# Optimization experiments

Measured on AMD Instinct MI355X. Metric: run time of the kernel, lower is better.

## Reference

```python
import jax, jax.numpy as jnp
import numpy as np


def _dwconv(x, w, b):
    # depthwise conv, NCHW, kernel [C,1,k,k], SAME padding k//2
    k = w.shape[-1]
    p = k // 2
    out = jax.lax.conv_general_dilated(x, w, (1, 1), [(p, p), (p, p)],
                                       feature_group_count=x.shape[1])
    return out + b[None, :, None, None]


def _conv1x1(x, W, b):
    return jnp.einsum('oc,bchw->bohw', W, x) + b[None, :, None, None]


def _ca_weight(q, k):
    # q,k: [b,c,h,w] -> energy [b,h,w,h+w]
    eH = jnp.einsum('bchw,bcgw->bhwg', q, k)  # attend along H (column)
    eW = jnp.einsum('bchw,bchv->bhwv', q, k)  # attend along W (row)
    return jnp.concatenate([eH, eW], axis=3)


def _ca_map(att, v):
    # att: [b,h,w,h+w], v: [b,c,h,w]
    h = v.shape[2]
    outH = jnp.einsum('bcgw,bhwg->bchw', v, att[..., :h])
    outW = jnp.einsum('bchv,bhwv->bchw', v, att[..., h:])
    return outH + outW


def _cc_block(cnn, Wq, bq, Wk, bk, Wv, bv, gamma):
    q = _conv1x1(cnn, Wq, bq)
    k = _conv1x1(cnn, Wk, bk)
    v = _conv1x1(cnn, Wv, bv)
    att = jax.nn.softmax(_ca_weight(q, k), axis=1)  # softmax over H axis, as in torch F.softmax(energy, 1)
    return gamma * _ca_map(att, v) + cnn


def _ppeg(x, w7, b7, w5, b5, w3, b3, H, W):
    C = x.shape[1]
    cnn = x.T.reshape(1, C, H, W)
    out = _dwconv(cnn, w7, b7) + cnn + _dwconv(cnn, w5, b5) + _dwconv(cnn, w3, b3)
    return out.reshape(C, H * W).T  # [N, C]


def setup_inputs() -> dict:
    key = jax.random.key(0)
    N, DIM, HID, QK = 65536, 1024, 512, 64  # N = 256^2
    ks = jax.random.split(key, 26)
    s = 0.02
    inp = {
        'h0': jax.random.normal(ks[0], (N, DIM), jnp.float32),
        'w7': jax.random.normal(ks[1], (DIM, 1, 7, 7)) * s,
        'b7': jax.random.normal(ks[2], (DIM,)) * s,
        'w5': jax.random.normal(ks[3], (DIM, 1, 5, 5)) * s,
        'b5': jax.random.normal(ks[4], (DIM,)) * s,
        'w3': jax.random.normal(ks[5], (DIM, 1, 3, 3)) * s,
        'b3': jax.random.normal(ks[6], (DIM,)) * s,
        'W1': jax.random.normal(ks[7], (HID, DIM)) * s,
        'b1': jax.random.normal(ks[8], (HID,)) * s,
        'Wq': jax.random.normal(ks[9], (QK, HID)) * s,
        'bq': jax.random.normal(ks[10], (QK,)) * s,
        'Wk': jax.random.normal(ks[11], (QK, HID)) * s,
        'bk': jax.random.normal(ks[12], (QK,)) * s,
        'Wv': jax.random.normal(ks[13], (HID, HID)) * s,
        'bv': jax.random.normal(ks[14], (HID,)) * s,
        'gamma': jax.random.normal(ks[15], ()) * 0.5,
        'Wq1': jax.random.normal(ks[16], (QK, HID)) * s,
        'bq1': jax.random.normal(ks[17], (QK,)) * s,
        'Wk1': jax.random.normal(ks[18], (QK, HID)) * s,
        'bk1': jax.random.normal(ks[19], (QK,)) * s,
        'Wv1': jax.random.normal(ks[20], (HID, HID)) * s,
        'bv1': jax.random.normal(ks[21], (HID,)) * s,
        'gamma1': jax.random.normal(ks[22], ()) * 0.5,
        'Wfc': jax.random.normal(ks[23], (1, HID)) * s,
        'bfc': jax.random.normal(ks[24], (1,)) * s,
    }
    return inp


def reference(h0, w7, b7, w5, b5, w3, b3, W1, b1,
              Wq, bq, Wk, bk, Wv, bv, gamma,
              Wq1, bq1, Wk1, bk1, Wv1, bv1, gamma1, Wfc, bfc):
    N = h0.shape[0]
    side = int(np.ceil(np.sqrt(N)))
    pad = side * side - N
    h1 = jnp.concatenate([h0, h0[:pad]], axis=0) if pad > 0 else h0
    # PPEG positional encoding (multi-kernel depthwise conv)
    h1 = _ppeg(h1, w7, b7, w5, b5, w3, b3, side, side)
    # fc1: Linear(1024->512) + ReLU  (h1 already square -> second pad is no-op)
    h2 = jax.nn.relu(h1 @ W1.T + b1)  # [N, 512]
    # CCAttention (two criss-cross blocks + fc to 1 logit)
    cnn = h2.T.reshape(1, h2.shape[1], side, side)
    out = _cc_block(cnn, Wq, bq, Wk, bk, Wv, bv, gamma)
    out1 = _cc_block(out, Wq1, bq1, Wk1, bk1, Wv1, bv1, gamma1)
    out1 = out1.reshape(out1.shape[1], side * side).T  # [N, 512]
    logits = out1 @ Wfc.T + bfc  # [N, 1]
    A = jax.nn.softmax(logits.T, axis=1)  # [1, N] attention over instances
    return A
```

## Files before the change

kernel.cpp:

```cpp
#include <hip/hip_runtime.h>

#define HW 65536
#define SIDE 256

typedef __attribute__((ext_vector_type(8))) short short8v;
typedef __attribute__((ext_vector_type(4))) float f32x4;
typedef __attribute__((ext_vector_type(8))) ushort ushort8v;

__device__ __forceinline__ ushort f2bf(float f) {
  unsigned int u = __builtin_bit_cast(unsigned int, f);
  u = (u + 0x7fff + ((u >> 16) & 1)) >> 16;
  return (ushort)u;
}
__device__ __forceinline__ float bf2f(unsigned int u) {
  return __builtin_bit_cast(float, (u & 0xffffu) << 16);
}
__device__ __forceinline__ float bflo(unsigned int d) {
  return __builtin_bit_cast(float, d << 16);
}
__device__ __forceinline__ float bfhi(unsigned int d) {
  return __builtin_bit_cast(float, d & 0xffff0000u);
}
__device__ __forceinline__ void gld16(const void* g, void* l) {
  __builtin_amdgcn_global_load_lds(
      (const __attribute__((address_space(1))) void*)g,
      (__attribute__((address_space(3))) void*)l, 16, 0, 0);
}

__global__ __launch_bounds__(256) void k_prep(
    const float* __restrict__ W1, const float* __restrict__ Wv,
    const float* __restrict__ Wv1, const float* __restrict__ Wq,
    const float* __restrict__ Wk, const float* __restrict__ Wq1,
    const float* __restrict__ Wk1, const float* __restrict__ bq,
    const float* __restrict__ bk, const float* __restrict__ bq1,
    const float* __restrict__ bk1, const float* __restrict__ w7,
    const float* __restrict__ b7, const float* __restrict__ w5,
    const float* __restrict__ b5, const float* __restrict__ w3,
    const float* __restrict__ b3,
    ushort* __restrict__ W1b, ushort* __restrict__ Wvb,
    ushort* __restrict__ Wv1b, ushort* __restrict__ Wqkb,
    ushort* __restrict__ Wqk1b, float* __restrict__ bqk,
    float* __restrict__ bqk1, float* __restrict__ wc, float* __restrict__ bc) {
  const int i = blockIdx.x * 256 + threadIdx.x;
  if (i < 524288) { W1b[i] = f2bf(W1[i]); return; }
  if (i < 786432) { int j = i - 524288; Wvb[j] = f2bf(Wv[j]); return; }
  if (i < 1048576) { int j = i - 786432; Wv1b[j] = f2bf(Wv1[j]); return; }
  if (i < 1081344) { int j = i - 1048576; Wqkb[j] = f2bf(Wq[j]); return; }
  if (i < 1114112) { int j = i - 1081344; Wqkb[32768 + j] = f2bf(Wk[j]); return; }
  if (i < 1146880) { int j = i - 1114112; Wqk1b[j] = f2bf(Wq1[j]); return; }
  if (i < 1179648) { int j = i - 1146880; Wqk1b[32768 + j] = f2bf(Wk1[j]); return; }
  if (i < 1179904) {
    int j = i - 1179648;
    if (j < 64) bqk[j] = bq[j];
    else if (j < 128) bqk[j] = bk[j - 64];
    else if (j < 192) bqk1[j - 128] = bq1[j - 128];
    else bqk1[j - 128] = bk1[j - 192];
    return;
  }
  if (i < 1180928) {
    const int c = i - 1179904;
    float w[49];
#pragma unroll
    for (int t = 0; t < 49; t++) w[t] = w7[c * 49 + t];
    for (int dy = 0; dy < 5; dy++)
      for (int dx = 0; dx < 5; dx++)
        w[(dy + 1) * 7 + (dx + 1)] += w5[c * 25 + dy * 5 + dx];
    for (int dy = 0; dy < 3; dy++)
      for (int dx = 0; dx < 3; dx++)
        w[(dy + 2) * 7 + (dx + 2)] += w3[c * 9 + dy * 3 + dx];
    w[3 * 7 + 3] += 1.0f;
#pragma unroll
    for (int t = 0; t < 49; t++) wc[c * 49 + t] = w[t];
    bc[c] = b7[c] + b5[c] + b3[c];
  }
}

__global__ __launch_bounds__(256) void k_transpose_nc_v(
    const float* __restrict__ in, ushort* __restrict__ out) {
  __shared__ ushort t[64][64];
  const int c0 = blockIdx.x << 6, r0 = blockIdx.y << 6;
  const int tid = threadIdx.x;
#pragma unroll
  for (int p = 0; p < 2; p++) {
    const int r = (tid >> 3) + p * 32, c8 = tid & 7;
    const float4 f0 = *(const float4*)&in[(size_t)(r0 + r) * 1024 + c0 + c8 * 8];
    const float4 f1 = *(const float4*)&in[(size_t)(r0 + r) * 1024 + c0 + c8 * 8 + 4];
    ushort8v v;
    v[0] = f2bf(f0.x); v[1] = f2bf(f0.y); v[2] = f2bf(f0.z); v[3] = f2bf(f0.w);
    v[4] = f2bf(f1.x); v[5] = f2bf(f1.y); v[6] = f2bf(f1.z); v[7] = f2bf(f1.w);
    *(ushort8v*)&t[r][(c8 ^ ((r >> 3) & 7)) * 8] = v;
  }
  __syncthreads();
#pragma unroll
  for (int p = 0; p < 2; p++) {
    const int c = (tid >> 3) + p * 32, r8 = tid & 7;
    ushort8v v;
#pragma unroll
    for (int j = 0; j < 8; j++) {
      const int rr = r8 * 8 + j;
      v[j] = t[rr][(((c >> 3) ^ r8) << 3) + (c & 7)];
    }
    *(ushort8v*)&out[(size_t)(c0 + c) * HW + r0 + r8 * 8] = v;
  }
}

__global__ __launch_bounds__(256) void k_trv(const ushort* __restrict__ in,
    ushort* __restrict__ out, int R, int C, long long bs) {
  __shared__ ushort t[64][64];
  const size_t base = (size_t)blockIdx.z * bs;
  const int c0 = blockIdx.x << 6, r0 = blockIdx.y << 6;
  const int tid = threadIdx.x;
#pragma unroll
  for (int p = 0; p < 2; p++) {
    const int r = (tid >> 3) + p * 32, c8 = tid & 7;
    const ushort8v v = *(const ushort8v*)&in[base + (size_t)(r0 + r) * C + c0 + c8 * 8];
    *(ushort8v*)&t[r][(c8 ^ ((r >> 3) & 7)) * 8] = v;
  }
  __syncthreads();
#pragma unroll
  for (int p = 0; p < 2; p++) {
    const int c = (tid >> 3) + p * 32, r8 = tid & 7;
    ushort8v v;
#pragma unroll
    for (int j = 0; j < 8; j++) {
      const int rr = r8 * 8 + j;
      v[j] = t[rr][(((c >> 3) ^ r8) << 3) + (c & 7)];
    }
    *(ushort8v*)&out[base + (size_t)(c0 + c) * R + r0 + r8 * 8] = v;
  }
}

__global__ __launch_bounds__(256) void k_dwconv7(const ushort* __restrict__ X,
    const float* __restrict__ wc, const float* __restrict__ bc,
    ushort* __restrict__ out) {
  __shared__ ushort tile[38][272];
  const int c = blockIdx.y;
  const int y0 = blockIdx.x << 5;
  const int tid = threadIdx.x;
  const ushort* Xc = X + (size_t)c * HW;

  float w[49];
#pragma unroll
  for (int i = 0; i < 49; i++) w[i] = wc[c * 49 + i];
  const float bcv = bc[c];

  if (tid < 76) {
    const int r = tid >> 1;
    ushort8v z = {0, 0, 0, 0, 0, 0, 0, 0};
    *(ushort8v*)&tile[r][(tid & 1) ? 264 : 0] = z;
  }
  for (int i = tid; i < 38 * 32; i += 256) {
    const int r = i >> 5, j8 = i & 31;
    const int y = y0 - 3 + r;
    ushort8v v = {0, 0, 0, 0, 0, 0, 0, 0};
    if (y >= 0 && y < SIDE) v = *(const ushort8v*)&Xc[y * SIDE + j8 * 8];
    *(ushort8v*)&tile[r][8 + j8 * 8] = v;
  }
  __syncthreads();

  const int t0 = tid & 63;
  const int ry = (tid >> 6) << 3;
  float acc[8][4] = {};
#pragma unroll
  for (int r = 0; r < 14; r++) {
    const uint2 ua = *(const uint2*)&tile[ry + r][(t0 << 2) + 4];
    const uint2 ub = *(const uint2*)&tile[ry + r][(t0 << 2) + 8];
    const uint2 uc = *(const uint2*)&tile[ry + r][(t0 << 2) + 12];
    float rv[12];
    rv[0] = bflo(ua.x); rv[1] = bfhi(ua.x); rv[2] = bflo(ua.y); rv[3] = bfhi(ua.y);
    rv[4] = bflo(ub.x); rv[5] = bfhi(ub.x); rv[6] = bflo(ub.y); rv[7] = bfhi(ub.y);
    rv[8] = bflo(uc.x); rv[9] = bfhi(uc.x); rv[10] = bflo(uc.y); rv[11] = bfhi(uc.y);
#pragma unroll
    for (int m = 0; m < 8; m++) {
      const int dy = r - m;
      if (dy < 0 || dy > 6) continue;
#pragma unroll
      for (int dx = 0; dx < 7; dx++) {
        const float ww = w[dy * 7 + dx];
#pragma unroll
        for (int o = 0; o < 4; o++) acc[m][o] += ww * rv[o + 1 + dx];
      }
    }
  }
#pragma unroll
  for (int m = 0; m < 8; m++) {
    ushort4 o4 = {f2bf(acc[m][0] + bcv), f2bf(acc[m][1] + bcv),
                  f2bf(acc[m][2] + bcv), f2bf(acc[m][3] + bcv)};
    *(ushort4*)&out[(size_t)c * HW + (y0 + ry + m) * SIDE + (t0 << 2)] = o4;
  }
}

template <int K, int RELU, int TRN>
__global__ __launch_bounds__(512) void k_mm8(
    const ushort* __restrict__ A, int lda,
    const ushort* __restrict__ B, int ldb,
    const float* __restrict__ bias,
    ushort* __restrict__ Cb, int ldc,
    ushort* __restrict__ Ct, int ldt) {
  constexpr int NT = K / 32;
  __shared__ __align__(16) ushort SM[2 * 12288];
  const int tid = threadIdx.x;
  const int lane = tid & 63, wv = tid >> 6;

  const int id = blockIdx.x;
  const int wg = (id & 7) * 128 + (id >> 3);
  const int bm = (wg >> 9) << 8;
  const int bn = (wg & 511) << 7;

  const int l4 = lane >> 2;
  const int sch = (lane & 3) ^ (l4 & 3);
  const int rA0 = (wv * 2) * 16 + l4;
  const int rA1 = (wv * 2 + 1) * 16 + l4;
  const int rB = wv * 16 + l4;
  const ushort* ApS0 = A + (size_t)(bm + rA0) * lda + sch * 8;
  const ushort* ApS1 = A + (size_t)(bm + rA1) * lda + sch * 8;
  const ushort* BpS = B + (size_t)(bn + rB) * ldb + sch * 8;
  const int dA0 = (wv * 2) * 512 + lane * 8;
  const int dA1 = (wv * 2 + 1) * 512 + lane * 8;
  const int dB = wv * 512 + lane * 8;

  const int wm = wv & 3, wn = wv >> 2;
  const int fr = lane & 15, kq = lane >> 4;
  int offA[4], offB[4];
#pragma unroll
  for (int mi = 0; mi < 4; mi++) {
    const int row = wm * 64 + mi * 16 + fr;
    offA[mi] = row * 32 + ((kq ^ (row & 3)) << 3);
  }
#pragma unroll
  for (int ni = 0; ni < 4; ni++) {
    const int row = wn * 64 + ni * 16 + fr;
    offB[ni] = 8192 + row * 32 + ((kq ^ (row & 3)) << 3);
  }

  f32x4 acc[4][4];
#pragma unroll
  for (int mi = 0; mi < 4; mi++)
#pragma unroll
    for (int ni = 0; ni < 4; ni++) acc[mi][ni] = (f32x4){0.f, 0.f, 0.f, 0.f};

#define STAGE8(bufbase, k0)                         \
  do {                                              \
    gld16(ApS0 + (k0), &SM[(bufbase) + dA0]);       \
    gld16(ApS1 + (k0), &SM[(bufbase) + dA1]);       \
    gld16(BpS + (k0), &SM[(bufbase) + 8192 + dB]);  \
  } while (0)

  STAGE8(0, 0);
  STAGE8(12288, 32);
  asm volatile("s_waitcnt vmcnt(3)" ::: "memory");
  __builtin_amdgcn_s_barrier();

  int cur = 0;
#pragma unroll 2
  for (int t = 0; t < NT; ++t) {
    const int base = cur ? 12288 : 0;
    short8v a[4], b2[4];
#pragma unroll
    for (int mi = 0; mi < 4; mi++) a[mi] = *(const short8v*)&SM[base + offA[mi]];
#pragma unroll
    for (int ni = 0; ni < 4; ni++) b2[ni] = *(const short8v*)&SM[base + offB[ni]];
    asm volatile("s_waitcnt lgkmcnt(0)" ::: "memory");
    __builtin_amdgcn_s_barrier();
    const int ts = (t + 2 < NT) ? (t + 2) : (NT - 1);
    STAGE8(base, ts << 5);
    __builtin_amdgcn_s_setprio(1);
#pragma unroll
    for (int mi = 0; mi < 4; mi++)
#pragma unroll
      for (int ni = 0; ni < 4; ni++)
        acc[mi][ni] = __builtin_amdgcn_mfma_f32_16x16x32_bf16(b2[ni], a[mi], acc[mi][ni], 0, 0, 0);
    __builtin_amdgcn_s_setprio(0);
    asm volatile("s_waitcnt vmcnt(3)" ::: "memory");
    __builtin_amdgcn_s_barrier();
    cur ^= 1;
  }
#undef STAGE8
  asm volatile("s_waitcnt vmcnt(0)" ::: "memory");
  __builtin_amdgcn_s_barrier();

  ushort tb[4][4][4];
#pragma unroll
  for (int mi = 0; mi < 4; mi++) {
    const int row = bm + wm * 64 + mi * 16 + fr;
    const float bs1 = bias[row];
#pragma unroll
    for (int ni = 0; ni < 4; ni++) {
      const int col = bn + wn * 64 + ni * 16 + (kq << 2);
      float4 v;
      v.x = acc[mi][ni][0] + bs1; v.y = acc[mi][ni][1] + bs1;
      v.z = acc[mi][ni][2] + bs1; v.w = acc[mi][ni][3] + bs1;
      if (RELU) {
        v.x = fmaxf(v.x, 0.f); v.y = fmaxf(v.y, 0.f);
        v.z = fmaxf(v.z, 0.f); v.w = fmaxf(v.w, 0.f);
      }
      const ushort4 u = {f2bf(v.x), f2bf(v.y), f2bf(v.z), f2bf(v.w)};
      *(ushort4*)&Cb[(size_t)row * ldc + col] = u;
      if (TRN) {
        tb[mi][ni][0] = u.x; tb[mi][ni][1] = u.y;
        tb[mi][ni][2] = u.z; tb[mi][ni][3] = u.w;
      }
    }
  }

  if constexpr (TRN) {
    ushort* St = SM;
#pragma unroll
    for (int hh = 0; hh < 2; hh++) {
      __builtin_amdgcn_s_barrier();
      if (wn == hh) {
#pragma unroll
        for (int mi = 0; mi < 4; mi++) {
          const int cl = wm * 64 + mi * 16 + fr;
#pragma unroll
          for (int ni = 0; ni < 4; ni++) {
            const int nl = ni * 16 + (kq << 2);
#pragma unroll
            for (int r = 0; r < 4; r++) St[(nl + r) * 256 + cl] = tb[mi][ni][r];
          }
        }
      }
      __builtin_amdgcn_s_barrier();
      const int cid = tid * 4;
      const int rowo = cid >> 5;
#pragma unroll
      for (int j = 0; j < 4; j++) {
        const int ch = (cid + j) & 31;
        const ushort8v vv = *(const ushort8v*)&St[rowo * 256 + ch * 8];
        *(ushort8v*)&Ct[(size_t)(bn + hh * 64 + rowo) * ldt + bm + ch * 8] = vv;
      }
    }
  }
}

template <int BN, int BIAS, int RELU, int OUTF, int OUTB, int SWZ>
__global__ __launch_bounds__(256) void k_mm(
    const ushort* __restrict__ A, int lda, long long bsA,
    const ushort* __restrict__ B, int ldb, long long bsB,
    const float* __restrict__ bias,
    float* __restrict__ Cf, ushort* __restrict__ Cb, int ldc, long long bsC,
    int K) {
  static_assert(BN == 64 || BN == 128, "BN");
  constexpr int FN = BN / 32;
  __shared__ __align__(16) ushort SMEM[128 * 32 + BN * 32];
  ushort* As = SMEM;
  ushort* Bs = SMEM + 128 * 32;
  const int tid = threadIdx.x;

  int bx, by, bz;
  if constexpr (SWZ == 0) {
    bx = blockIdx.x; by = blockIdx.y; bz = blockIdx.z;
  } else if constexpr (SWZ == 2) {
    const int id = blockIdx.x, l = id >> 3;
    bz = (id & 7) * 32 + (l >> 2); bx = l & 1; by = (l >> 1) & 1;
  } else {
    const int id = blockIdx.x, l = id >> 3;
    bz = (id & 7) * 32 + (l >> 3); bx = l & 3; by = (l >> 2) & 1;
  }

  const int bm = bx << 7, bn = by * BN;
  const long long zA = (long long)bz * bsA;
  const long long zB = (long long)bz * bsB;
  const long long zC = (long long)bz * bsC;

  const int sr = tid >> 2, sq = tid & 3;
  const int sw0 = (sr >> 1) & 3;
  const int sw1 = ((sr + 64) >> 1) & 3;
  const ushort* Ap0 = A + zA + (size_t)(bm + sr) * lda + ((sq ^ sw0) << 3);
  const ushort* Ap1 = A + zA + (size_t)(bm + sr + 64) * lda + ((sq ^ sw1) << 3);
  const ushort* Bp0 = B + zB + (size_t)(bn + sr) * ldb + ((sq ^ sw0) << 3);
  const ushort* Bp1 = nullptr;
  if constexpr (BN == 128)
    Bp1 = B + zB + (size_t)(bn + sr + 64) * ldb + ((sq ^ sw1) << 3);
  ushort* wA0 = &As[sr * 32 + sq * 8];
  ushort* wA1 = &As[(sr + 64) * 32 + sq * 8];
  ushort* wB0 = &Bs[sr * 32 + sq * 8];
  ushort* wB1 = nullptr;
  if constexpr (BN == 128) wB1 = &Bs[(sr + 64) * 32 + sq * 8];

  const int lane = tid & 63, wv = tid >> 6;
  const int wm = wv & 1, wn = wv >> 1;
  const int fr = lane & 15, kq = lane >> 4;
  int offA[4], offB[FN];
#pragma unroll
  for (int mi = 0; mi < 4; mi++) {
    const int row = wm * 64 + mi * 16 + fr;
    offA[mi] = row * 32 + ((kq ^ ((row >> 1) & 3)) << 3);
  }
#pragma unroll
  for (int ni = 0; ni < FN; ni++) {
    const int row = wn * (BN / 2) + ni * 16 + fr;
    offB[ni] = row * 32 + ((kq ^ ((row >> 1) & 3)) << 3);
  }

  f32x4 acc[4][FN];
#pragma unroll
  for (int mi = 0; mi < 4; mi++)
#pragma unroll
    for (int ni = 0; ni < FN; ni++) acc[mi][ni] = (f32x4){0.f, 0.f, 0.f, 0.f};

  for (int k0 = 0; k0 < K; k0 += 32) {
    __syncthreads();
    gld16(Ap0 + k0, wA0);
    gld16(Ap1 + k0, wA1);
    gld16(Bp0 + k0, wB0);
    if constexpr (BN == 128) gld16(Bp1 + k0, wB1);
    __syncthreads();
    short8v a[4], b[FN];
#pragma unroll
    for (int mi = 0; mi < 4; mi++) a[mi] = *(const short8v*)&As[offA[mi]];
#pragma unroll
    for (int ni = 0; ni < FN; ni++) b[ni] = *(const short8v*)&Bs[offB[ni]];
#pragma unroll
    for (int mi = 0; mi < 4; mi++)
#pragma unroll
      for (int ni = 0; ni < FN; ni++)
        acc[mi][ni] = __builtin_amdgcn_mfma_f32_16x16x32_bf16(b[ni], a[mi], acc[mi][ni], 0, 0, 0);
  }

#pragma unroll
  for (int mi = 0; mi < 4; mi++) {
    const int row = bm + wm * 64 + mi * 16 + fr;
    const float bs1 = (BIAS == 1) ? bias[row] : 0.f;
#pragma unroll
    for (int ni = 0; ni < FN; ni++) {
      const int col = bn + wn * (BN / 2) + ni * 16 + (kq << 2);
      float4 v;
      v.x = acc[mi][ni][0]; v.y = acc[mi][ni][1];
      v.z = acc[mi][ni][2]; v.w = acc[mi][ni][3];
      if (BIAS == 1) { v.x += bs1; v.y += bs1; v.z += bs1; v.w += bs1; }
      if (BIAS == 2) {
        const float4 bc4 = *(const float4*)&bias[col];
        v.x += bc4.x; v.y += bc4.y; v.z += bc4.z; v.w += bc4.w;
      }
      if (RELU) {
        v.x = fmaxf(v.x, 0.f); v.y = fmaxf(v.y, 0.f);
        v.z = fmaxf(v.z, 0.f); v.w = fmaxf(v.w, 0.f);
      }
      const size_t idx = (size_t)(zC + (size_t)row * ldc + col);
      if (OUTF) *(float4*)&Cf[idx] = v;
      if (OUTB) {
        ushort4 u = {f2bf(v.x), f2bf(v.y), f2bf(v.z), f2bf(v.w)};
        *(ushort4*)&Cb[idx] = u;
      }
    }
  }
}

__global__ __launch_bounds__(256) void k_energy(
    const ushort* __restrict__ A, int lda, long long bsA,
    const ushort* __restrict__ B, int ldb, long long bsB,
    ushort* __restrict__ E) {
  __shared__ __align__(16) ushort SA[128 * 64];
  __shared__ __align__(16) ushort SB[128 * 64];
  const int tid = threadIdx.x;
  const int id = blockIdx.x, l = id >> 3;
  const int bz = (id & 7) * 32 + (l >> 2), bx = l & 1, by = (l >> 1) & 1;
  const int bm = bx << 7, bn = by << 7;
  const long long zA = (long long)bz * bsA;
  const long long zB = (long long)bz * bsB;

#pragma unroll
  for (int j = 0; j < 4; j++) {
    const int g = j * 256 + tid;
    const int row = g >> 3, ch = g & 7;
    const int sc = ch ^ (row & 7);
    gld16(A + zA + (size_t)(bm + row) * lda + sc * 8, &SA[g * 8]);
    gld16(B + zB + (size_t)(bn + row) * ldb + sc * 8, &SB[g * 8]);
  }
  __syncthreads();

  const int lane = tid & 63, wv = tid >> 6;
  const int wm = wv & 1, wn = wv >> 1;
  const int fr = lane & 15, kq = lane >> 4;
  f32x4 acc[4][4];
#pragma unroll
  for (int mi = 0; mi < 4; mi++)
#pragma unroll
    for (int ni = 0; ni < 4; ni++) acc[mi][ni] = (f32x4){0.f, 0.f, 0.f, 0.f};

#pragma unroll
  for (int ks = 0; ks < 2; ks++) {
    short8v a[4], b[4];
#pragma unroll
    for (int mi = 0; mi < 4; mi++) {
      const int row = wm * 64 + mi * 16 + fr;
      a[mi] = *(const short8v*)&SA[row * 64 + (((ks * 4 + kq) ^ (row & 7)) << 3)];
    }
#pragma unroll
    for (int ni = 0; ni < 4; ni++) {
      const int row = wn * 64 + ni * 16 + fr;
      b[ni] = *(const short8v*)&SB[row * 64 + (((ks * 4 + kq) ^ (row & 7)) << 3)];
    }
#pragma unroll
    for (int mi = 0; mi < 4; mi++)
#pragma unroll
      for (int ni = 0; ni < 4; ni++)
        acc[mi][ni] = __builtin_amdgcn_mfma_f32_16x16x32_bf16(b[ni], a[mi], acc[mi][ni], 0, 0, 0);
  }

  const long long zC = (long long)bz * 65536;
#pragma unroll
  for (int mi = 0; mi < 4; mi++) {
    const int row = bm + wm * 64 + mi * 16 + fr;
#pragma unroll
    for (int ni = 0; ni < 4; ni++) {
      const int col = bn + wn * 64 + ni * 16 + (kq << 2);
      ushort4 u = {f2bf(acc[mi][ni][0]), f2bf(acc[mi][ni][1]),
                   f2bf(acc[mi][ni][2]), f2bf(acc[mi][ni][3])};
      *(ushort4*)&E[(size_t)(zC + (size_t)row * 256 + col)] = u;
    }
  }
}

__global__ __launch_bounds__(256) void k_softmax8(const ushort* __restrict__ EW,
    ushort* __restrict__ AW, const ushort* __restrict__ EH,
    ushort* __restrict__ AH) {
  __shared__ float sm[8][32], ss[8][32];
  const int b = blockIdx.x, tid = threadIdx.x;
  const int lc = tid & 31, seg = tid >> 5;
  const ushort* E;
  ushort* A;
  size_t base;
  int hs;
  if (b < 2048) {
    E = EW; A = AW; hs = HW;
    base = (size_t)b * 32 + lc;
  } else {
    E = EH; A = AH; hs = 256;
    const int cf = (b - 2048) * 32 + lc;
    base = (size_t)(cf >> 8) * HW + (cf & 255);
  }
  const size_t bh = base + (size_t)(seg * 32) * hs;
  float v[32];
#pragma unroll
  for (int h = 0; h < 32; h++) v[h] = bf2f(E[bh + (size_t)h * hs]);
  float m = v[0];
#pragma unroll
  for (int h = 1; h < 32; h++) m = fmaxf(m, v[h]);
  float s = 0.f;
#pragma unroll
  for (int h = 0; h < 32; h++) s += __expf(v[h] - m);
  sm[seg][lc] = m;
  ss[seg][lc] = s;
  __syncthreads();
  float M = sm[0][lc];
#pragma unroll
  for (int i = 1; i < 8; i++) M = fmaxf(M, sm[i][lc]);
  float S = 0.f;
#pragma unroll
  for (int i = 0; i < 8; i++) S += ss[i][lc] * __expf(sm[i][lc] - M);
  const float inv = 1.0f / S;
#pragma unroll
  for (int h = 0; h < 32; h++)
    A[bh + (size_t)h * hs] = f2bf(__expf(v[h] - M) * inv);
}

__global__ __launch_bounds__(256) void k_merge3(const ushort* __restrict__ O,
    const ushort* __restrict__ TH, const ushort* __restrict__ CN,
    const float* __restrict__ gammap, ushort* __restrict__ outB) {
  __shared__ ushort t[64][64];
  const float g = *gammap;
  const size_t base = (size_t)blockIdx.z * HW;
  const int h0 = blockIdx.y << 6, w0 = blockIdx.x << 6;
  const int tid = threadIdx.x;
#pragma unroll
  for (int p = 0; p < 2; p++) {
    const int r = (tid >> 3) + p * 32, c8 = tid & 7;
    const ushort8v v = *(const ushort8v*)&TH[base + (w0 + r) * SIDE + h0 + c8 * 8];
    *(ushort8v*)&t[r][(c8 ^ ((r >> 3) & 7)) * 8] = v;
  }
  __syncthreads();
#pragma unroll
  for (int p = 0; p < 2; p++) {
    const int h = (tid >> 3) + p * 32, r8 = tid & 7;
    const size_t idx = base + (h0 + h) * SIDE + w0 + r8 * 8;
    const ushort8v o8 = *(const ushort8v*)&O[idx];
    const ushort8v c8v = *(const ushort8v*)&CN[idx];
    ushort8v res;
#pragma unroll
    for (int j = 0; j < 8; j++) {
      const int rr = r8 * 8 + j;
      const float th = bf2f(t[rr][(((h >> 3) ^ r8) << 3) + (h & 7)]);
      res[j] = f2bf(g * (bf2f(o8[j]) + th) + bf2f(c8v[j]));
    }
    *(ushort8v*)&outB[idx] = res;
  }
}

__global__ __launch_bounds__(256) void k_logits2(const ushort* __restrict__ X,
    const float* __restrict__ Wfc, const float* __restrict__ bfc,
    float* __restrict__ L) {
  const int n0 = (blockIdx.x * 256 + threadIdx.x) * 2;
  float s0 = 0.f, s1 = 0.f;
  for (int j = 0; j < 512; j++) {
    const unsigned int u = *(const unsigned int*)&X[(size_t)j * HW + n0];
    const float wj = Wfc[j];
    s0 += bflo(u) * wj;
    s1 += bfhi(u) * wj;
  }
  float2 o = {s0 + bfc[0], s1 + bfc[0]};
  *(float2*)&L[n0] = o;
}

__global__ __launch_bounds__(256) void k_smax_reduce(const float* __restrict__ L,
                                                     float* __restrict__ red) {
  __shared__ float sm[256];
  const int tid = threadIdx.x;
  float m = -3.4e38f;
  for (int i = tid; i < HW; i += 256) m = fmaxf(m, L[i]);
  sm[tid] = m;
  __syncthreads();
  for (int s = 128; s > 0; s >>= 1) {
    if (tid < s) sm[tid] = fmaxf(sm[tid], sm[tid + s]);
    __syncthreads();
  }
  const float M = sm[0];
  __syncthreads();
  float sum = 0.f;
  for (int i = tid; i < HW; i += 256) sum += expf(L[i] - M);
  sm[tid] = sum;
  __syncthreads();
  for (int s = 128; s > 0; s >>= 1) {
    if (tid < s) sm[tid] += sm[tid + s];
    __syncthreads();
  }
  if (tid == 0) { red[0] = M; red[1] = sm[0]; }
}

__global__ __launch_bounds__(256) void k_smax_write(const float* __restrict__ L,
    const float* __restrict__ red, float* __restrict__ out) {
  const int n = blockIdx.x * 256 + threadIdx.x;
  out[n] = expf(L[n] - red[0]) * (1.0f / red[1]);
}

extern "C" void kernel_launch(void* const* d_in, const int* in_sizes, int n_in,
                              void* d_out, int out_size, void* d_ws, size_t ws_size,
                              hipStream_t stream) {
  const float* h0 = (const float*)d_in[0];
  const float* w7 = (const float*)d_in[1];
  const float* b7 = (const float*)d_in[2];
  const float* w5 = (const float*)d_in[3];
  const float* b5 = (const float*)d_in[4];
  const float* w3 = (const float*)d_in[5];
  const float* b3 = (const float*)d_in[6];
  const float* W1 = (const float*)d_in[7];
  const float* b1 = (const float*)d_in[8];
  const float* Wq = (const float*)d_in[9];
  const float* bq = (const float*)d_in[10];
  const float* Wk = (const float*)d_in[11];
  const float* bk = (const float*)d_in[12];
  const float* Wv = (const float*)d_in[13];
  const float* bv = (const float*)d_in[14];
  const float* gamma = (const float*)d_in[15];
  const float* Wq1 = (const float*)d_in[16];
  const float* bq1 = (const float*)d_in[17];
  const float* Wk1 = (const float*)d_in[18];
  const float* bk1 = (const float*)d_in[19];
  const float* Wv1 = (const float*)d_in[20];
  const float* bv1 = (const float*)d_in[21];
  const float* gamma1 = (const float*)d_in[22];
  const float* Wfc = (const float*)d_in[23];
  const float* bfc = (const float*)d_in[24];

  char* W = (char*)d_ws;
  const size_t MB = 1 << 20;
  ushort* Xb    = (ushort*)(W + 0);
  ushort* H2b   = (ushort*)(W + 0);
  ushort* H2t   = (ushort*)(W + 64 * MB);
  ushort* qkt   = (ushort*)(W + 128 * MB);
  ushort* AttW  = (ushort*)(W + 144 * MB);
  ushort* AttH  = (ushort*)(W + 176 * MB);
  ushort* H1b   = (ushort*)(W + 256 * MB);
  ushort* H1t   = (ushort*)(W + 384 * MB);
  ushort* Vb    = (ushort*)(W + 384 * MB);
  ushort* vTb   = (ushort*)(W + 448 * MB);
  ushort* Ob    = (ushort*)(W + 512 * MB);
  ushort* THbb  = (ushort*)(W + 576 * MB);
  ushort* EbW   = (ushort*)(W + 640 * MB);
  ushort* EbH   = (ushort*)(W + 672 * MB);
  ushort* W1b   = (ushort*)(W + 704 * MB);
  ushort* Wvb   = (ushort*)(W + 705 * MB);
  ushort* Wv1b  = (ushort*)(W + 705 * MB + 512 * 1024);
  ushort* Wqkb  = (ushort*)(W + 706 * MB);
  ushort* Wqk1b = (ushort*)(W + 706 * MB + 128 * 1024);
  float*  wcomb = (float*)(W + 706 * MB + 256 * 1024);
  float*  bcomb = (float*)(W + 706 * MB + 464 * 1024);
  float*  bqk   = (float*)(W + 706 * MB + 472 * 1024);
  float*  bqk1  = (float*)(W + 706 * MB + 474 * 1024);
  float*  L     = (float*)(W + 707 * MB);
  float*  red   = (float*)(W + 707 * MB + 256 * 1024);

  k_prep<<<4613, 256, 0, stream>>>(W1, Wv, Wv1, Wq, Wk, Wq1, Wk1,
                                   bq, bk, bq1, bk1, w7, b7, w5, b5, w3, b3,
                                   W1b, Wvb, Wv1b, Wqkb, Wqk1b, bqk, bqk1,
                                   wcomb, bcomb);

  k_transpose_nc_v<<<dim3(16, 1024), 256, 0, stream>>>(h0, Xb);
  k_dwconv7<<<dim3(8, 1024), 256, 0, stream>>>(Xb, wcomb, bcomb, H1b);
  k_trv<<<dim3(1024, 16, 1), 256, 0, stream>>>(H1b, H1t, 1024, HW, 0);

  k_mm8<1024, 1, 1><<<1024, 512, 0, stream>>>(
      W1b, 1024, H1t, 1024, b1, H2b, HW, H2t, 512);

  auto cc_block = [&](const ushort* act, ushort* cnn, const ushort* Wqk_,
                      const float* bqk_, const ushort* Wv_, const float* bv_,
                      const float* gam) {
    k_mm<128, 2, 0, 0, 1, 0><<<dim3(512, 1, 1), 256, 0, stream>>>(
        act, 512, 0, Wqk_, 512, 0, bqk_, nullptr, qkt, 128, 0, 512);
    k_mm8<512, 0, 0><<<1024, 512, 0, stream>>>(
        Wv_, 512, act, 512, bv_, Vb, HW, nullptr, 0);
    k_trv<<<dim3(4, 4, 512), 256, 0, stream>>>(Vb, vTb, 256, 256, 65536);
    k_energy<<<1024, 256, 0, stream>>>(qkt, 128, 32768, qkt + 64, 128, 32768, EbW);
    k_energy<<<1024, 256, 0, stream>>>(qkt, 32768, 128, qkt + 64, 32768, 128, EbH);
    k_softmax8<<<4096, 256, 0, stream>>>(EbW, AttW, EbH, AttH);
    k_mm<128, 0, 0, 0, 1, 3><<<2048, 256, 0, stream>>>(
        Vb, HW, 256, AttW, 256, 65536, nullptr, nullptr, Ob, HW, 256, 256);
    k_mm<128, 0, 0, 0, 1, 3><<<2048, 256, 0, stream>>>(
        vTb, HW, 256, AttH, 256, 65536, nullptr, nullptr, THbb, HW, 256, 256);
    k_merge3<<<dim3(4, 4, 512), 256, 0, stream>>>(Ob, THbb, cnn, gam, cnn);
  };

  cc_block(H2t, H2b, Wqkb, bqk, Wvb, bv, gamma);
  k_trv<<<dim3(1024, 8, 1), 256, 0, stream>>>(H2b, H2t, 512, HW, 0);
  cc_block(H2t, H2b, Wqk1b, bqk1, Wv1b, bv1, gamma1);

  k_logits2<<<128, 256, 0, stream>>>(H2b, Wfc, bfc, L);
  k_smax_reduce<<<1, 256, 0, stream>>>(L, red);
  k_smax_write<<<256, 256, 0, stream>>>(L, red, (float*)d_out);
}
```

Before: 1.184 ms.

## Run PPEG depthwise conv directly in NHWC layout, dropping both transposes

Replaces the transpose-to-NCHW, per-channel depthwise conv and transpose-back pipeline with a plain fp32-to-bf16 cast and a new depthwise conv that works on NHWC data. Each block handles a 16x16 spatial tile for 16 channels, with the combined weights relaid out per channel group. The output goes straight into the [N,1024] layout the fc1 GEMM reads. This removes two full transpose passes over the 128MB activation. In exchange, the conv now does strided 8-byte global loads and stages the tile in fp32 in LDS, which may reduce load efficiency.

```diff
diff --git a/kernel.cpp b/kernel.cpp
--- a/kernel.cpp
+++ b/kernel.cpp
@@ -40,7 +40,7 @@
     ushort* __restrict__ W1b, ushort* __restrict__ Wvb,
     ushort* __restrict__ Wv1b, ushort* __restrict__ Wqkb,
     ushort* __restrict__ Wqk1b, float* __restrict__ bqk,
-    float* __restrict__ bqk1, float* __restrict__ wc, float* __restrict__ bc) {
+    float* __restrict__ bqk1, float* __restrict__ wc2, float* __restrict__ bc) {
   const int i = blockIdx.x * 256 + threadIdx.x;
   if (i < 524288) { W1b[i] = f2bf(W1[i]); return; }
   if (i < 786432) { int j = i - 524288; Wvb[j] = f2bf(Wv[j]); return; }
@@ -70,38 +70,83 @@
         w[(dy + 2) * 7 + (dx + 2)] += w3[c * 9 + dy * 3 + dx];
     w[3 * 7 + 3] += 1.0f;
 #pragma unroll
-    for (int t = 0; t < 49; t++) wc[c * 49 + t] = w[t];
+    for (int t = 0; t < 49; t++)
+      wc2[(c >> 4) * 784 + t * 16 + (c & 15)] = w[t];
     bc[c] = b7[c] + b5[c] + b3[c];
   }
 }
 
-__global__ __launch_bounds__(256) void k_transpose_nc_v(
-    const float* __restrict__ in, ushort* __restrict__ out) {
-  __shared__ ushort t[64][64];
-  const int c0 = blockIdx.x << 6, r0 = blockIdx.y << 6;
+__global__ __launch_bounds__(256) void k_cast16(const float* __restrict__ in,
+                                                ushort* __restrict__ out) {
+  const size_t base = ((size_t)blockIdx.x * 256 + threadIdx.x) * 16;
+  const float4 f0 = *(const float4*)&in[base];
+  const float4 f1 = *(const float4*)&in[base + 4];
+  const float4 f2 = *(const float4*)&in[base + 8];
+  const float4 f3 = *(const float4*)&in[base + 12];
+  ushort8v a, b;
+  a[0] = f2bf(f0.x); a[1] = f2bf(f0.y); a[2] = f2bf(f0.z); a[3] = f2bf(f0.w);
+  a[4] = f2bf(f1.x); a[5] = f2bf(f1.y); a[6] = f2bf(f1.z); a[7] = f2bf(f1.w);
+  b[0] = f2bf(f2.x); b[1] = f2bf(f2.y); b[2] = f2bf(f2.z); b[3] = f2bf(f2.w);
+  b[4] = f2bf(f3.x); b[5] = f2bf(f3.y); b[6] = f2bf(f3.z); b[7] = f2bf(f3.w);
+  *(ushort8v*)&out[base] = a;
+  *(ushort8v*)&out[base + 8] = b;
+}
+
+__global__ __launch_bounds__(256) void k_dwconv_nhwc(
+    const ushort* __restrict__ Xn, const float* __restrict__ wc2,
+    const float* __restrict__ bc, ushort* __restrict__ out) {
+  __shared__ float tile[484 * 20];
+  const int xt = blockIdx.x << 4, yt = blockIdx.y << 4;
+  const int cg = blockIdx.z;
+  const int c0 = cg << 4;
   const int tid = threadIdx.x;
-#pragma unroll
-  for (int p = 0; p < 2; p++) {
-    const int r = (tid >> 3) + p * 32, c8 = tid & 7;
-    const float4 f0 = *(const float4*)&in[(size_t)(r0 + r) * 1024 + c0 + c8 * 8];
-    const float4 f1 = *(const float4*)&in[(size_t)(r0 + r) * 1024 + c0 + c8 * 8 + 4];
-    ushort8v v;
-    v[0] = f2bf(f0.x); v[1] = f2bf(f0.y); v[2] = f2bf(f0.z); v[3] = f2bf(f0.w);
-    v[4] = f2bf(f1.x); v[5] = f2bf(f1.y); v[6] = f2bf(f1.z); v[7] = f2bf(f1.w);
-    *(ushort8v*)&t[r][(c8 ^ ((r >> 3) & 7)) * 8] = v;
+
+  for (int g = tid; g < 484 * 4; g += 256) {
+    const int p = g >> 2, q = g & 3;
+    const int r = p / 22, s = p - r * 22;
+    const int gy = yt - 3 + r, gx = xt - 3 + s;
+    float4 f = {0.f, 0.f, 0.f, 0.f};
+    if (gy >= 0 && gy < SIDE && gx >= 0 && gx < SIDE) {
+      const uint2 u = *(const uint2*)&Xn[(size_t)(gy * SIDE + gx) * 1024 + c0 + q * 4];
+      f.x = bflo(u.x); f.y = bfhi(u.x);
+      f.z = bflo(u.y); f.w = bfhi(u.y);
+    }
+    *(float4*)&tile[p * 20 + q * 4] = f;
   }
   __syncthreads();
-#pragma unroll
-  for (int p = 0; p < 2; p++) {
-    const int c = (tid >> 3) + p * 32, r8 = tid & 7;
-    ushort8v v;
-#pragma unroll
-    for (int j = 0; j < 8; j++) {
-      const int rr = r8 * 8 + j;
-      v[j] = t[rr][(((c >> 3) ^ r8) << 3) + (c & 7)];
-    }
-    *(ushort8v*)&out[(size_t)(c0 + c) * HW + r0 + r8 * 8] = v;
-  }
+
+  const int tx = tid & 15, ty = tid >> 4;
+  const float* wg = wc2 + cg * 784;
+  float acc[16] = {};
+#pragma unroll
+  for (int dy = 0; dy < 7; dy++) {
+#pragma unroll
+    for (int dx = 0; dx < 7; dx++) {
+      const int p = (ty + dy) * 22 + (tx + dx);
+      const float* wt = wg + (dy * 7 + dx) * 16;
+      const float4 i0 = *(const float4*)&tile[p * 20];
+      const float4 i1 = *(const float4*)&tile[p * 20 + 4];
+      const float4 i2 = *(const float4*)&tile[p * 20 + 8];
+      const float4 i3 = *(const float4*)&tile[p * 20 + 12];
+      acc[0] += wt[0] * i0.x;  acc[1] += wt[1] * i0.y;
+      acc[2] += wt[2] * i0.z;  acc[3] += wt[3] * i0.w;
+      acc[4] += wt[4] * i1.x;  acc[5] += wt[5] * i1.y;
+      acc[6] += wt[6] * i1.z;  acc[7] += wt[7] * i1.w;
+      acc[8] += wt[8] * i2.x;  acc[9] += wt[9] * i2.y;
+      acc[10] += wt[10] * i2.z; acc[11] += wt[11] * i2.w;
+      acc[12] += wt[12] * i3.x; acc[13] += wt[13] * i3.y;
+      acc[14] += wt[14] * i3.z; acc[15] += wt[15] * i3.w;
+    }
+  }
+  const int n = (yt + ty) * SIDE + (xt + tx);
+  ushort8v o0, o1;
+#pragma unroll
+  for (int j = 0; j < 8; j++) {
+    o0[j] = f2bf(acc[j] + bc[c0 + j]);
+    o1[j] = f2bf(acc[8 + j] + bc[c0 + 8 + j]);
+  }
+  *(ushort8v*)&out[(size_t)n * 1024 + c0] = o0;
+  *(ushort8v*)&out[(size_t)n * 1024 + c0 + 8] = o1;
 }
 
 __global__ __launch_bounds__(256) void k_trv(const ushort* __restrict__ in,
@@ -127,66 +172,6 @@
       v[j] = t[rr][(((c >> 3) ^ r8) << 3) + (c & 7)];
     }
     *(ushort8v*)&out[base + (size_t)(c0 + c) * R + r0 + r8 * 8] = v;
-  }
-}
-
-__global__ __launch_bounds__(256) void k_dwconv7(const ushort* __restrict__ X,
-    const float* __restrict__ wc, const float* __restrict__ bc,
-    ushort* __restrict__ out) {
-  __shared__ ushort tile[38][272];
-  const int c = blockIdx.y;
-  const int y0 = blockIdx.x << 5;
-  const int tid = threadIdx.x;
-  const ushort* Xc = X + (size_t)c * HW;
-
-  float w[49];
-#pragma unroll
-  for (int i = 0; i < 49; i++) w[i] = wc[c * 49 + i];
-  const float bcv = bc[c];
-
-  if (tid < 76) {
-    const int r = tid >> 1;
-    ushort8v z = {0, 0, 0, 0, 0, 0, 0, 0};
-    *(ushort8v*)&tile[r][(tid & 1) ? 264 : 0] = z;
-  }
-  for (int i = tid; i < 38 * 32; i += 256) {
-    const int r = i >> 5, j8 = i & 31;
-    const int y = y0 - 3 + r;
-    ushort8v v = {0, 0, 0, 0, 0, 0, 0, 0};
-    if (y >= 0 && y < SIDE) v = *(const ushort8v*)&Xc[y * SIDE + j8 * 8];
-    *(ushort8v*)&tile[r][8 + j8 * 8] = v;
-  }
-  __syncthreads();
-
-  const int t0 = tid & 63;
-  const int ry = (tid >> 6) << 3;
-  float acc[8][4] = {};
-#pragma unroll
-  for (int r = 0; r < 14; r++) {
-    const uint2 ua = *(const uint2*)&tile[ry + r][(t0 << 2) + 4];
-    const uint2 ub = *(const uint2*)&tile[ry + r][(t0 << 2) + 8];
-    const uint2 uc = *(const uint2*)&tile[ry + r][(t0 << 2) + 12];
-    float rv[12];
-    rv[0] = bflo(ua.x); rv[1] = bfhi(ua.x); rv[2] = bflo(ua.y); rv[3] = bfhi(ua.y);
-    rv[4] = bflo(ub.x); rv[5] = bfhi(ub.x); rv[6] = bflo(ub.y); rv[7] = bfhi(ub.y);
-    rv[8] = bflo(uc.x); rv[9] = bfhi(uc.x); rv[10] = bflo(uc.y); rv[11] = bfhi(uc.y);
-#pragma unroll
-    for (int m = 0; m < 8; m++) {
-      const int dy = r - m;
-      if (dy < 0 || dy > 6) continue;
-#pragma unroll
-      for (int dx = 0; dx < 7; dx++) {
-        const float ww = w[dy * 7 + dx];
-#pragma unroll
-        for (int o = 0; o < 4; o++) acc[m][o] += ww * rv[o + 1 + dx];
-      }
-    }
-  }
-#pragma unroll
-  for (int m = 0; m < 8; m++) {
-    ushort4 o4 = {f2bf(acc[m][0] + bcv), f2bf(acc[m][1] + bcv),
-                  f2bf(acc[m][2] + bcv), f2bf(acc[m][3] + bcv)};
-    *(ushort4*)&out[(size_t)c * HW + (y0 + ry + m) * SIDE + (t0 << 2)] = o4;
   }
 }
 
@@ -665,16 +650,15 @@
 
   char* W = (char*)d_ws;
   const size_t MB = 1 << 20;
-  ushort* Xb    = (ushort*)(W + 0);
+  ushort* Xn    = (ushort*)(W + 0);
   ushort* H2b   = (ushort*)(W + 0);
   ushort* H2t   = (ushort*)(W + 64 * MB);
   ushort* qkt   = (ushort*)(W + 128 * MB);
   ushort* AttW  = (ushort*)(W + 144 * MB);
   ushort* AttH  = (ushort*)(W + 176 * MB);
-  ushort* H1b   = (ushort*)(W + 256 * MB);
   ushort* H1t   = (ushort*)(W + 384 * MB);
-  ushort* Vb    = (ushort*)(W + 384 * MB);
-  ushort* vTb   = (ushort*)(W + 448 * MB);
+  ushort* Vb    = (ushort*)(W + 256 * MB);
+  ushort* vTb   = (ushort*)(W + 320 * MB);
   ushort* Ob    = (ushort*)(W + 512 * MB);
   ushort* THbb  = (ushort*)(W + 576 * MB);
   ushort* EbW   = (ushort*)(W + 640 * MB);
@@ -684,7 +668,7 @@
   ushort* Wv1b  = (ushort*)(W + 705 * MB + 512 * 1024);
   ushort* Wqkb  = (ushort*)(W + 706 * MB);
   ushort* Wqk1b = (ushort*)(W + 706 * MB + 128 * 1024);
-  float*  wcomb = (float*)(W + 706 * MB + 256 * 1024);
+  float*  wcomb2 = (float*)(W + 706 * MB + 256 * 1024);
   float*  bcomb = (float*)(W + 706 * MB + 464 * 1024);
   float*  bqk   = (float*)(W + 706 * MB + 472 * 1024);
   float*  bqk1  = (float*)(W + 706 * MB + 474 * 1024);
@@ -694,11 +678,10 @@
   k_prep<<<4613, 256, 0, stream>>>(W1, Wv, Wv1, Wq, Wk, Wq1, Wk1,
                                    bq, bk, bq1, bk1, w7, b7, w5, b5, w3, b3,
                                    W1b, Wvb, Wv1b, Wqkb, Wqk1b, bqk, bqk1,
-                                   wcomb, bcomb);
-
-  k_transpose_nc_v<<<dim3(16, 1024), 256, 0, stream>>>(h0, Xb);
-  k_dwconv7<<<dim3(8, 1024), 256, 0, stream>>>(Xb, wcomb, bcomb, H1b);
-  k_trv<<<dim3(1024, 16, 1), 256, 0, stream>>>(H1b, H1t, 1024, HW, 0);
+                                   wcomb2, bcomb);
+
+  k_cast16<<<16384, 256, 0, stream>>>(h0, Xn);
+  k_dwconv_nhwc<<<dim3(16, 16, 64), 256, 0, stream>>>(Xn, wcomb2, bcomb, H1t);
 
   k_mm8<1024, 1, 1><<<1024, 512, 0, stream>>>(
       W1b, 1024, H1t, 1024, b1, H2b, HW, H2t, 512);
```

New measurement: 1.225 ms. 1.04x slower.
